# Kernel optimization log

Measured on AMD Instinct MI355X. Metric: run time of the kernel, lower is better.

The kernel has to match this reference:

```python
import jax, jax.numpy as jnp
import numpy as np

NUM_CODES = 1024
CODE_DIM = 64
N_TOKENS = 131072
DECAY = 0.99
EPS = 1e-5


def setup_inputs() -> dict:
    key = jax.random.key(0)
    k1, k2, k3, k4 = jax.random.split(key, 4)
    return {
        "z": jax.random.normal(k1, (N_TOKENS, CODE_DIM), dtype=jnp.float32),
        "codebook": jax.random.normal(k2, (NUM_CODES, CODE_DIM), dtype=jnp.float32),
        "cluster_size": jax.random.uniform(k3, (NUM_CODES,), dtype=jnp.float32),
        "ema_w": jax.random.normal(k4, (NUM_CODES, CODE_DIM), dtype=jnp.float32),
    }


def reference(z, codebook, cluster_size, ema_w):
    # Squared L2 distances; argmin over squared distances == argmin over cdist.
    # d2: [N, K]
    d2 = (
        jnp.sum(z * z, axis=-1, keepdims=True)
        - 2.0 * (z @ codebook.T)
        + jnp.sum(codebook * codebook, axis=-1)
    )
    indices = jnp.argmin(d2, axis=-1)          # [N] int
    quantized = codebook[indices]              # [N, D]

    # EMA statistics (torch version uses one_hot; segment_sum is the fused
    # equivalent without materializing the [N, K] one-hot matrix).
    counts = jax.ops.segment_sum(jnp.ones_like(indices, dtype=z.dtype), indices,
                                 num_segments=NUM_CODES)          # encodings.sum(0)
    dw = jax.ops.segment_sum(z, indices, num_segments=NUM_CODES)  # encodings.T @ z

    new_cluster_size = DECAY * cluster_size + (1.0 - DECAY) * counts
    new_ema_w = DECAY * ema_w + (1.0 - DECAY) * dw
    n = jnp.sum(new_cluster_size)
    cs = (new_cluster_size + EPS) / (n + NUM_CODES * EPS) * n
    new_codebook = new_ema_w / cs[:, None]

    commitment_loss = jnp.mean((z - jax.lax.stop_gradient(quantized)) ** 2)
    quantized_st = z + jax.lax.stop_gradient(quantized - z)  # straight-through

    return quantized_st, indices, commitment_loss, new_codebook, new_cluster_size, new_ema_w
```

## Files before the change

kernel.cpp:

```cpp
#include <hip/hip_runtime.h>
#include <hip/hip_bf16.h>


#define DECAY 0.99f
#define OMD   0.01f
#define EPSV  1e-5f
#define BIASF 192.0f

typedef __attribute__((ext_vector_type(8))) __bf16 bf16x8;
typedef __attribute__((ext_vector_type(4))) float  float4v;

static __device__ __forceinline__ bf16x8 cvt8(float4v a, float4v b) {
    bf16x8 r;
    r[0] = (__bf16)a[0]; r[1] = (__bf16)a[1]; r[2] = (__bf16)a[2]; r[3] = (__bf16)a[3];
    r[4] = (__bf16)b[0]; r[5] = (__bf16)b[1]; r[6] = (__bf16)b[2]; r[7] = (__bf16)b[3];
    return r;
}

static __device__ __forceinline__ int dec_idx(unsigned key, int quad) {
    int iter = key & 255;
    return ((iter >> 6) << 8) + (((iter >> 2) & 15) << 4) + (quad << 2) + (iter & 3);
}

__global__ void vq_prep(const float* __restrict__ cb,
                        float* __restrict__ wsf, int* __restrict__ wsi,
                        unsigned short* __restrict__ pk,
                        int K, int NT) {
    int t = blockIdx.x * 256 + threadIdx.x;
    if (t < K) {
        wsi[t] = 0;
        const float4v* cp = (const float4v*)(cb + (size_t)t * 64);
        float s = 0.f;
        #pragma unroll
        for (int i = 0; i < 16; ++i) {
            float4v v = cp[i];
            s += v[0] * v[0] + v[1] * v[1] + v[2] * v[2] + v[3] * v[3];
        }
        wsf[K + t] = BIASF - 0.5f * s;
    }
    if (t < K * 4) {
        int tg  = t >> 6;
        int l   = t & 63;
        int col = l & 15, q = l >> 4;
        int code = tg * 16 + col;
        bf16x8 a0, a1;
        if (code < K) {
            const float* s0 = cb + (size_t)code * 64 + q * 8;
            a0 = cvt8(*(const float4v*)(s0),      *(const float4v*)(s0 + 4));
            a1 = cvt8(*(const float4v*)(s0 + 32), *(const float4v*)(s0 + 36));
        } else {
            #pragma unroll
            for (int j = 0; j < 8; ++j) { a0[j] = (__bf16)0.f; a1[j] = (__bf16)0.f; }
        }
        bf16x8* dst = (bf16x8*)(pk + (size_t)t * 16);
        dst[0] = a0;
        dst[1] = a1;
    }
    if (t == 0) wsf[2 * K] = 0.f;
}

__launch_bounds__(512)
__global__ void vq_main(const float* __restrict__ z,
                        const float* __restrict__ cb,
                        const unsigned short* __restrict__ pk,
                        float* __restrict__ wsf, int* __restrict__ wsi,
                        float* __restrict__ out,
                        int NT, int K) {
    __shared__ int hist[1024];

    const int tid  = threadIdx.x;
    const int lane = tid & 63;
    const int col  = lane & 15;
    const int quad = lane >> 4;
    const int wtok0 = blockIdx.x * 256 + (tid >> 6) * 32;
    const float* cnormp = wsf + K;
    float* lossp = wsf + 2 * K;
    const bool smallK = (K <= 1024);

    for (int i = tid; i < 1024; i += 512) hist[i] = 0;

    bf16x8 bf0[2], bf1[2];
    #pragma unroll
    for (int g = 0; g < 2; ++g) {
        int tok = wtok0 + g * 16 + col;
        if (tok >= NT) tok = NT - 1;
        const float* zp = z + (size_t)tok * 64 + quad * 8;
        bf0[g] = cvt8(*(const float4v*)(zp),      *(const float4v*)(zp + 4));
        bf1[g] = cvt8(*(const float4v*)(zp + 32), *(const float4v*)(zp + 36));
    }

    unsigned k1[2] = { 0u, 0u }, k2[2] = { 0u, 0u };
    const unsigned kmask = 0xFFFFFF00u;
    const int ngrp = (K + 15) >> 4;
    const unsigned short* pl = pk + lane * 16;

    #pragma unroll 2
    for (int tt = 0; tt < ngrp; ++tt) {
        const bf16x8* frag = (const bf16x8*)(pl + (size_t)tt * 1024);
        bf16x8 a0 = frag[0];
        bf16x8 a1 = frag[1];
        float4v cni = *(const float4v*)(cnormp + tt * 16 + quad * 4);
        const int iterbase = tt << 2;
        #pragma unroll
        for (int g = 0; g < 2; ++g) {
            float4v acc = cni;
            acc = __builtin_amdgcn_mfma_f32_16x16x32_bf16(a0, bf0[g], acc, 0, 0, 0);
            acc = __builtin_amdgcn_mfma_f32_16x16x32_bf16(a1, bf1[g], acc, 0, 0, 0);
            #pragma unroll
            for (int r = 0; r < 4; ++r) {
                unsigned kb = (__float_as_uint(acc[r]) & kmask) | (unsigned)(iterbase + r);
                unsigned lo = k2[g] > kb ? k2[g] : kb;
                k2[g] = k1[g] < lo ? k1[g] : lo;
                k1[g] = k1[g] > kb ? k1[g] : kb;
            }
        }
    }

    int ibst[2];
    #pragma unroll
    for (int g = 0; g < 2; ++g) {
        int tok = wtok0 + g * 16 + col;
        if (tok >= NT) tok = NT - 1;
        int ia = dec_idx(k1[g], quad);
        int ib = dec_idx(k2[g], quad);
        int cand[8];
        #pragma unroll
        for (int q = 0; q < 4; ++q) {
            cand[2 * q]     = __shfl(ia, q * 16 + col, 64);
            cand[2 * q + 1] = __shfl(ib, q * 16 + col, 64);
        }
        const float* zr = z + (size_t)tok * 64 + quad * 16;
        float4v zv0 = *(const float4v*)(zr);
        float4v zv1 = *(const float4v*)(zr + 4);
        float4v zv2 = *(const float4v*)(zr + 8);
        float4v zv3 = *(const float4v*)(zr + 12);
        double ps[8];
        #pragma unroll
        for (int s = 0; s < 8; ++s) {
            int cc = (cand[s] < K) ? cand[s] : 0;
            const float* cr = cb + (size_t)cc * 64 + quad * 16;
            float4v c0 = *(const float4v*)(cr);
            float4v c1 = *(const float4v*)(cr + 4);
            float4v c2 = *(const float4v*)(cr + 8);
            float4v c3 = *(const float4v*)(cr + 12);
            double a = 0.0;
            #pragma unroll
            for (int j = 0; j < 4; ++j) {
                double e0 = (double)zv0[j] - (double)c0[j];
                double e1 = (double)zv1[j] - (double)c1[j];
                double e2 = (double)zv2[j] - (double)c2[j];
                double e3 = (double)zv3[j] - (double)c3[j];
                a = fma(e0, e0, a); a = fma(e1, e1, a);
                a = fma(e2, e2, a); a = fma(e3, e3, a);
            }
            ps[s] = (cand[s] < K) ? a : 1.0e300;
        }
        #pragma unroll
        for (int s = 0; s < 8; ++s) {
            ps[s] += __shfl_xor(ps[s], 16, 64);
            ps[s] += __shfl_xor(ps[s], 32, 64);
        }
        double bs = ps[0]; int bi = cand[0];
        #pragma unroll
        for (int s = 1; s < 8; ++s) {
            if (ps[s] < bs || (ps[s] == bs && cand[s] < bi)) { bs = ps[s]; bi = cand[s]; }
        }
        ibst[g] = bi;
    }

    const size_t off_idx = (size_t)NT * 64;
    __syncthreads();

    if (lane < 32) {
        int tk = wtok0 + lane;
        if (tk < NT) {
            int ib = (lane < 16) ? ibst[0] : ibst[1];
            out[off_idx + tk] = (float)ib;
            if (smallK) atomicAdd(&hist[ib], 1);
            else        atomicAdd(&wsi[ib], 1);
        }
    }

    float lsum = 0.f;
    #pragma unroll
    for (int i = 0; i < 8; ++i) {
        int tw  = i * 4 + quad;
        int g   = i >> 2;
        int idx = __shfl(ibst[g], tw & 15, 64);
        int token = wtok0 + tw;
        if (token < NT) {
            int d4 = col * 4;
            float4v zf = *(const float4v*)(z  + (size_t)token * 64 + d4);
            float4v qf = *(const float4v*)(cb + (size_t)idx   * 64 + d4);
            *(float4v*)(out + (size_t)token * 64 + d4) = qf;
            float e0 = zf[0] - qf[0], e1 = zf[1] - qf[1];
            float e2 = zf[2] - qf[2], e3 = zf[3] - qf[3];
            lsum += e0 * e0 + e1 * e1 + e2 * e2 + e3 * e3;
        }
    }
    #pragma unroll
    for (int off = 1; off < 64; off <<= 1) lsum += __shfl_xor(lsum, off, 64);
    if (lane == 0) atomicAdd(lossp, lsum);

    __syncthreads();
    if (smallK) {
        for (int k = tid; k < K; k += 512) {
            int c = hist[k];
            if (c) atomicAdd(&wsi[k], c);
        }
    }
}

__launch_bounds__(512)
__global__ void vq_dwred(const float* __restrict__ z,
                         const float* __restrict__ out_idx,
                         const float* __restrict__ cs,
                         float* __restrict__ wsf, const int* __restrict__ wsi,
                         float* __restrict__ partial,
                         float* __restrict__ out,
                         int NT, int K, int nchunks) {
    extern __shared__ float acc[];
    __shared__ float red[8];

    const int tid   = threadIdx.x;
    const int lane  = tid & 63;
    const int wave  = tid >> 6;
    const int chunk = blockIdx.x >> 2;
    const int g     = blockIdx.x & 3;
    const int tsub  = lane >> 4;
    const int d     = lane & 15;
    const size_t KD = (size_t)K * 64;

    for (int i = tid; i < K * 16; i += 512) acc[i] = 0.f;

    if (blockIdx.x == 0) {
        float part = 0.f;
        for (int k = tid; k < K; k += 512)
            part += DECAY * cs[k] + OMD * (float)wsi[k];
        #pragma unroll
        for (int off = 1; off < 64; off <<= 1) part += __shfl_xor(part, off, 64);
        if (lane == 0) red[wave] = part;
        __syncthreads();
        if (tid == 0) {
            float nn = 0.f;
            #pragma unroll
            for (int i = 0; i < 8; ++i) nn += red[i];
            wsf[2 * K + 1] = nn;
            out[(size_t)NT * 64 + NT] = wsf[2 * K] / ((float)NT * 64.0f);
        }
    }
    __syncthreads();

    const int C  = (NT + nchunks - 1) / nchunks;
    const int T0 = chunk * C;
    const int T1 = (T0 + C < NT) ? (T0 + C) : NT;
    const float* zs = z + g * 16 + d;

    #pragma unroll 4
    for (int t = T0 + wave * 4 + tsub; t < T1; t += 32) {
        float v   = zs[(size_t)t * 64];
        int  code = (int)out_idx[t];
        atomicAdd(&acc[code * 16 + d], v);
    }
    __syncthreads();

    float* pb = partial + (size_t)chunk * KD + g * 16;
    for (int i = tid; i < K * 16; i += 512) {
        int k = i >> 4, dd = i & 15;
        pb[(size_t)k * 64 + dd] = acc[i];
    }
}

__global__ void vq_final(const float* __restrict__ cs,
                         const float* __restrict__ ema,
                         const float* __restrict__ wsf,
                         const int* __restrict__ wsi,
                         const float* __restrict__ partial,
                         float* __restrict__ out, int NT, int K, int S) {
    const int KD = K * 64;
    int t = blockIdx.x * 256 + threadIdx.x;
    if (t >= KD) return;
    const int k = t >> 6;
    const float n = wsf[2 * K + 1];
    float dsum = 0.f;
    #pragma unroll 4
    for (int s = 0; s < S; ++s) dsum += partial[(size_t)s * KD + t];
    const float dw = DECAY * ema[t] + OMD * dsum;
    const float ncs = DECAY * cs[k] + OMD * (float)wsi[k];
    const float csn = (ncs + EPSV) / (n + (float)K * EPSV) * n;
    const size_t off_cb  = (size_t)NT * 64 + NT + 1;
    const size_t off_cs  = off_cb + (size_t)KD;
    const size_t off_ema = off_cs + K;
    out[off_cb  + t] = dw / csn;
    out[off_ema + t] = dw;
    if ((t & 63) == 0) out[off_cs + k] = ncs;
}

extern "C" void kernel_launch(void* const* d_in, const int* in_sizes, int n_in,
                              void* d_out, int out_size, void* d_ws, size_t ws_size,
                              hipStream_t stream) {
    const float* z   = (const float*)d_in[0];
    const float* cb  = (const float*)d_in[1];
    const float* cs  = (const float*)d_in[2];
    const float* ema = (const float*)d_in[3];
    float* out = (float*)d_out;
    float* wsf = (float*)d_ws;
    int*   wsi = (int*)d_ws;

    const int NT = in_sizes[0] / 64;
    const int K  = in_sizes[2];
    const int KD = K * 64;

    const size_t off_pk = (((size_t)2 * K + 2) + 7) & ~(size_t)7;
    const size_t off_pa = off_pk + (size_t)K * 32;

    size_t avail = ws_size / 4;
    int nchunks = 128;
    while (nchunks > 1 && off_pa + (size_t)nchunks * KD > avail)
        nchunks >>= 1;

    unsigned short* pk = (unsigned short*)(wsf + off_pk);
    float* partial = wsf + off_pa;
    const size_t dwlds = (size_t)K * 16 * sizeof(float);

    vq_prep<<<(K * 4 + 255) / 256, 256, 0, stream>>>(cb, wsf, wsi, pk, K, NT);
    vq_main<<<(NT + 255) / 256, 512, 0, stream>>>(z, cb, pk, wsf, wsi, out, NT, K);
    vq_dwred<<<nchunks * 4, 512, dwlds, stream>>>(
        z, out + (size_t)NT * 64, cs, wsf, wsi, partial, out, NT, K, nchunks);
    vq_final<<<(KD + 255) / 256, 256, 0, stream>>>(cs, ema, wsf, wsi, partial,
                                                   out, NT, K, nchunks);
}
```

Baseline: 255.8 us.

## Halve tokens per wave, prefetch next codebook fragment, raise occupancy

Each wave now handles 16 tokens instead of 32. That halves the per-wave accumulator and key registers, and the grid doubles to 128 tokens per block. The codebook fragment and norm loads for the next group are software-prefetched one iteration ahead. Launch bounds now request 8 waves per EU. The aim is to hide global-load latency in the distance loop through higher occupancy and prefetching. The cost is that each codebook fragment is reused across only one MFMA token group, so codebook traffic per token doubles.

Measured after the change: 347.3 us. 35.8% more time.

```diff
diff --git a/kernel.cpp b/kernel.cpp
--- a/kernel.cpp
+++ b/kernel.cpp
@@ -59,7 +59,7 @@
     if (t == 0) wsf[2 * K] = 0.f;
 }
 
-__launch_bounds__(512)
+__launch_bounds__(512, 8)
 __global__ void vq_main(const float* __restrict__ z,
                         const float* __restrict__ cb,
                         const unsigned short* __restrict__ pk,
@@ -72,57 +72,59 @@
     const int lane = tid & 63;
     const int col  = lane & 15;
     const int quad = lane >> 4;
-    const int wtok0 = blockIdx.x * 256 + (tid >> 6) * 32;
+    const int wtok0 = blockIdx.x * 128 + (tid >> 6) * 16;
     const float* cnormp = wsf + K;
     float* lossp = wsf + 2 * K;
     const bool smallK = (K <= 1024);
 
     for (int i = tid; i < 1024; i += 512) hist[i] = 0;
 
-    bf16x8 bf0[2], bf1[2];
-    #pragma unroll
-    for (int g = 0; g < 2; ++g) {
-        int tok = wtok0 + g * 16 + col;
+    bf16x8 bf0, bf1;
+    {
+        int tok = wtok0 + col;
         if (tok >= NT) tok = NT - 1;
         const float* zp = z + (size_t)tok * 64 + quad * 8;
-        bf0[g] = cvt8(*(const float4v*)(zp),      *(const float4v*)(zp + 4));
-        bf1[g] = cvt8(*(const float4v*)(zp + 32), *(const float4v*)(zp + 36));
-    }
-
-    unsigned k1[2] = { 0u, 0u }, k2[2] = { 0u, 0u };
+        bf0 = cvt8(*(const float4v*)(zp),      *(const float4v*)(zp + 4));
+        bf1 = cvt8(*(const float4v*)(zp + 32), *(const float4v*)(zp + 36));
+    }
+
+    unsigned k1 = 0u, k2 = 0u;
     const unsigned kmask = 0xFFFFFF00u;
     const int ngrp = (K + 15) >> 4;
     const unsigned short* pl = pk + lane * 16;
 
+    bf16x8 a0 = ((const bf16x8*)pl)[0];
+    bf16x8 a1 = ((const bf16x8*)pl)[1];
+    float4v cni = *(const float4v*)(cnormp + quad * 4);
+
     #pragma unroll 2
     for (int tt = 0; tt < ngrp; ++tt) {
-        const bf16x8* frag = (const bf16x8*)(pl + (size_t)tt * 1024);
-        bf16x8 a0 = frag[0];
-        bf16x8 a1 = frag[1];
-        float4v cni = *(const float4v*)(cnormp + tt * 16 + quad * 4);
+        const int ttn = (tt + 1 < ngrp) ? tt + 1 : tt;
+        const bf16x8* f = (const bf16x8*)(pl + (size_t)ttn * 1024);
+        bf16x8 n0 = f[0];
+        bf16x8 n1 = f[1];
+        float4v cnn = *(const float4v*)(cnormp + ttn * 16 + quad * 4);
+
+        float4v acc = cni;
+        acc = __builtin_amdgcn_mfma_f32_16x16x32_bf16(a0, bf0, acc, 0, 0, 0);
+        acc = __builtin_amdgcn_mfma_f32_16x16x32_bf16(a1, bf1, acc, 0, 0, 0);
         const int iterbase = tt << 2;
         #pragma unroll
-        for (int g = 0; g < 2; ++g) {
-            float4v acc = cni;
-            acc = __builtin_amdgcn_mfma_f32_16x16x32_bf16(a0, bf0[g], acc, 0, 0, 0);
-            acc = __builtin_amdgcn_mfma_f32_16x16x32_bf16(a1, bf1[g], acc, 0, 0, 0);
-            #pragma unroll
-            for (int r = 0; r < 4; ++r) {
-                unsigned kb = (__float_as_uint(acc[r]) & kmask) | (unsigned)(iterbase + r);
-                unsigned lo = k2[g] > kb ? k2[g] : kb;
-                k2[g] = k1[g] < lo ? k1[g] : lo;
-                k1[g] = k1[g] > kb ? k1[g] : kb;
-            }
-        }
-    }
-
-    int ibst[2];
-    #pragma unroll
-    for (int g = 0; g < 2; ++g) {
-        int tok = wtok0 + g * 16 + col;
+        for (int r = 0; r < 4; ++r) {
+            unsigned kb = (__float_as_uint(acc[r]) & kmask) | (unsigned)(iterbase + r);
+            unsigned lo = k2 > kb ? k2 : kb;
+            k2 = k1 < lo ? k1 : lo;
+            k1 = k1 > kb ? k1 : kb;
+        }
+        a0 = n0; a1 = n1; cni = cnn;
+    }
+
+    int ibst;
+    {
+        int tok = wtok0 + col;
         if (tok >= NT) tok = NT - 1;
-        int ia = dec_idx(k1[g], quad);
-        int ib = dec_idx(k2[g], quad);
+        int ia = dec_idx(k1, quad);
+        int ib = dec_idx(k2, quad);
         int cand[8];
         #pragma unroll
         for (int q = 0; q < 4; ++q) {
@@ -165,28 +167,26 @@
         for (int s = 1; s < 8; ++s) {
             if (ps[s] < bs || (ps[s] == bs && cand[s] < bi)) { bs = ps[s]; bi = cand[s]; }
         }
-        ibst[g] = bi;
+        ibst = bi;
     }
 
     const size_t off_idx = (size_t)NT * 64;
     __syncthreads();
 
-    if (lane < 32) {
+    if (lane < 16) {
         int tk = wtok0 + lane;
         if (tk < NT) {
-            int ib = (lane < 16) ? ibst[0] : ibst[1];
-            out[off_idx + tk] = (float)ib;
-            if (smallK) atomicAdd(&hist[ib], 1);
-            else        atomicAdd(&wsi[ib], 1);
+            out[off_idx + tk] = (float)ibst;
+            if (smallK) atomicAdd(&hist[ibst], 1);
+            else        atomicAdd(&wsi[ibst], 1);
         }
     }
 
     float lsum = 0.f;
     #pragma unroll
-    for (int i = 0; i < 8; ++i) {
+    for (int i = 0; i < 4; ++i) {
         int tw  = i * 4 + quad;
-        int g   = i >> 2;
-        int idx = __shfl(ibst[g], tw & 15, 64);
+        int idx = __shfl(ibst, tw, 64);
         int token = wtok0 + tw;
         if (token < NT) {
             int d4 = col * 4;
@@ -324,7 +324,7 @@
     const size_t dwlds = (size_t)K * 16 * sizeof(float);
 
     vq_prep<<<(K * 4 + 255) / 256, 256, 0, stream>>>(cb, wsf, wsi, pk, K, NT);
-    vq_main<<<(NT + 255) / 256, 512, 0, stream>>>(z, cb, pk, wsf, wsi, out, NT, K);
+    vq_main<<<(NT + 127) / 128, 512, 0, stream>>>(z, cb, pk, wsf, wsi, out, NT, K);
     vq_dwred<<<nchunks * 4, 512, dwlds, stream>>>(
         z, out + (size_t)NT * 64, cs, wsf, wsi, partial, out, NT, K, nchunks);
     vq_final<<<(KD + 255) / 256, 256, 0, stream>>>(cs, ema, wsf, wsi, partial,
```
